# Kernel tuning notes

Hardware: AMD Instinct MI355X
Metric: run time of the kernel (lower is better)

## Reference

```python
import jax, jax.numpy as jnp
import numpy as np

B, L, D = 8, 8192, 256
H = 4 * D
EPS_LN = 1e-5
EPS_RELU = 1e-6
MIN_A, MAX_A, OFFSET = 0, 3, 3


def setup_inputs() -> dict:
    key = jax.random.key(0)
    ks = jax.random.split(key, 6)
    def n(k, shape, s=0.02):
        return jax.random.normal(k, shape, jnp.float32) * s
    return {
        "x": jax.random.normal(ks[0], (B, L, D), jnp.float32),
        "g1": jnp.ones((D,), jnp.float32), "b1": jnp.zeros((D,), jnp.float32),
        "g2": jnp.ones((D,), jnp.float32), "b2": jnp.zeros((D,), jnp.float32),
        "filt_w": n(ks[1], (L, D)),
        "w1": n(ks[2], (D, H)), "bb1": jnp.zeros((H,), jnp.float32),
        "w2": n(ks[3], (H, D)), "bb2": jnp.zeros((D,), jnp.float32),
    }


def layernorm(x, g, b):
    m = jnp.mean(x, -1, keepdims=True)
    v = jnp.var(x, -1, keepdims=True)
    return (x - m) * jax.lax.rsqrt(v + EPS_LN) * g + b


def maxpool_same(x, w):
    # stride-1 max pool over the last (frequency) axis, SAME padding
    if w == 1:
        return x
    return jax.lax.reduce_window(x, -jnp.inf, jax.lax.max,
                                 (1, 1, w), (1, 1, 1), "SAME")


def spsd1d(xt):
    """SPSD1D: FFT-based multi-scale (alpha) max-pooling spectral filter.
    xt: (B, D, L). Keeps rfft bins that are local maxima at every scale
    2**alpha for alpha in [MIN_A, MAX_A]; the lowest OFFSET bins pass through.
    Returns filtered signal (B, D, L) and argmax-alpha holder (B, D, F)."""
    X = jnp.fft.rfft(xt, axis=-1)              # (B, D, F), F = L//2 + 1
    mag = jnp.abs(X)
    pooled = jnp.stack([maxpool_same(mag, 2 ** a)
                        for a in range(MIN_A, MAX_A + 1)], 0)  # (A, B, D, F)
    max_holder = jnp.argmax(pooled, axis=0)
    env = jnp.max(pooled, axis=0)
    keep = (mag >= env) | (jnp.arange(mag.shape[-1]) < OFFSET)
    Xf = jnp.where(keep, X, 0.0)
    out = jnp.fft.irfft(Xf, n=xt.shape[-1], axis=-1)
    return out, max_holder


def _block_forward(x, g1, b1, g2, b2, filt_w, w1, bb1, w2, bb2):
    # EpsilonReLU(LayerNorm(x))
    h = jax.nn.relu(layernorm(x, g1, b1)) + EPS_RELU      # (B, L, D)
    # GlobalSPSDFilter: spsd over sequence axis, then elementwise weight
    f, _max_holder = spsd1d(jnp.swapaxes(h, 1, 2))        # (B, D, L)
    x0 = jnp.swapaxes(f, 1, 2) * filt_w                   # (B, L, D)
    # MLP(LayerNorm(x0)); dropouts are identity in eval mode
    m = layernorm(x0, g2, b2)
    m = jax.nn.gelu(m @ w1 + bb1, approximate=False)
    x0 = m @ w2 + bb2
    return x + x0


def reference(x, g1, b1, g2, b2, filt_w, w1, bb1, w2, bb2):
    return _block_forward(x, g1, b1, g2, b2, filt_w, w1, bb1, w2, bb2)
```

## Files before the change

### kernel.cpp

```cpp
#include <hip/hip_runtime.h>
#include <hip/hip_bf16.h>

#define BSZ  8
#define LSEQ 8192
#define DDIM 256
#define HDIM 1024
#define MFFT 4096

typedef __bf16 bf16;
typedef __bf16 bf16x8 __attribute__((ext_vector_type(8)));
typedef __bf16 bf16x4 __attribute__((ext_vector_type(4)));
typedef float  f32x4  __attribute__((ext_vector_type(4)));

__device__ __forceinline__ void wave_reduce2(float& a, float& b) {
    #pragma unroll
    for (int off = 1; off < 64; off <<= 1) {
        a += __shfl_xor(a, off);
        b += __shfl_xor(b, off);
    }
}

__device__ __forceinline__ void gl_lds16(const void* g, void* l) {
    __builtin_amdgcn_global_load_lds(
        (const __attribute__((address_space(1))) unsigned int*)(unsigned long long)g,
        (__attribute__((address_space(3))) unsigned int*)(unsigned int)(unsigned long long)l,
        16, 0, 0);
}

__global__ __launch_bounds__(256) void k0_prep(const float* __restrict__ w1,
                                               const float* __restrict__ w2,
                                               bf16* __restrict__ w1k,
                                               bf16* __restrict__ w2k,
                                               float2* __restrict__ tbl) {
    const int e = blockIdx.x * 256 + threadIdx.x;
    {
        const int c = e >> 13, r = e & 8191;
        const int ks = r >> 10, grp = (r >> 8) & 3, hh = (r >> 3) & 31, j = r & 7;
        w1k[e] = (bf16)w1[(ks * 32 + grp * 8 + j) * HDIM + c * 32 + hh];
    }
    {
        const int c = e >> 13, r = e & 8191;
        const int grp = r >> 11, d = (r >> 3) & 255, j = r & 7;
        w2k[e] = (bf16)w2[(c * 32 + grp * 8 + j) * DDIM + d];
    }
    if (e <= 8184) {
        float ang;
        if (e < 3584) {
            const int f = e / 512 + 1, jj = e & 511;
            ang = -6.283185307179586f * (float)(f * jj) * (1.0f / 4096.0f);
        } else if (e < 4032) {
            const int t = e - 3584, f = t / 64 + 1, jj = t & 63;
            ang = -6.283185307179586f * (float)(f * jj) * (1.0f / 512.0f);
        } else if (e < 4088) {
            const int t = e - 4032, f = t / 8 + 1, jj = t & 7;
            ang = -6.283185307179586f * (float)(f * jj) * (1.0f / 64.0f);
        } else {
            const int k = e - 4088;
            ang = 3.14159265358979323846f * (float)k * (1.0f / 4096.0f);
        }
        tbl[e] = make_float2(cosf(ang), sinf(ang));
    }
}

__global__ __launch_bounds__(256) void k1_ln1_relu_T(const float* __restrict__ x,
                                                     const float* __restrict__ g1,
                                                     const float* __restrict__ b1,
                                                     float* __restrict__ ht) {
    __shared__ float tile[DDIM][33];
    const int tid  = threadIdx.x;
    const int wave = tid >> 6, lane = tid & 63;
    const int b  = blockIdx.x >> 8;
    const int l0 = (blockIdx.x & 255) << 5;
    const float4 g4 = *(const float4*)&g1[lane * 4];
    const float4 b4 = *(const float4*)&b1[lane * 4];
    for (int r8 = 0; r8 < 8; ++r8) {
        const int l = r8 * 4 + wave;
        const float4 v = *(const float4*)&x[(b * LSEQ + l0 + l) * DDIM + lane * 4];
        float s = v.x + v.y + v.z + v.w;
        float q = v.x * v.x + v.y * v.y + v.z * v.z + v.w * v.w;
        wave_reduce2(s, q);
        const float mean = s * (1.0f / 256.0f);
        const float var  = q * (1.0f / 256.0f) - mean * mean;
        const float rstd = rsqrtf(var + 1e-5f);
        const float vv[4] = {v.x, v.y, v.z, v.w};
        const float gg[4] = {g4.x, g4.y, g4.z, g4.w};
        const float bb[4] = {b4.x, b4.y, b4.z, b4.w};
        #pragma unroll
        for (int j = 0; j < 4; ++j) {
            float t = (vv[j] - mean) * rstd * gg[j] + bb[j];
            t = fmaxf(t, 0.0f) + 1e-6f;
            tile[lane * 4 + j][l] = t;
        }
    }
    __syncthreads();
    for (int i = tid; i < DDIM * 32; i += 256) {
        const int d = i >> 5, ll = i & 31;
        ht[(b * DDIM + d) * LSEQ + l0 + ll] = tile[d][ll];
    }
}

__device__ __forceinline__ int zs(int p) { return p ^ ((p >> 4) & 15); }
__device__ __forceinline__ float2 cmulf(float2 a, float2 b) {
    return make_float2(fmaf(a.x, b.x, -a.y * b.y), fmaf(a.x, b.y, a.y * b.x));
}
__device__ __forceinline__ float2 f2add(float2 a, float2 b) { return make_float2(a.x + b.x, a.y + b.y); }
__device__ __forceinline__ float2 f2sub(float2 a, float2 b) { return make_float2(a.x - b.x, a.y - b.y); }
#define CSQ2 0.70710678118654752440f

__device__ __forceinline__ void dft8(float2 a0, float2 a1, float2 a2, float2 a3,
                                     float2 a4, float2 a5, float2 a6, float2 a7,
                                     float2& y0, float2& y1, float2& y2, float2& y3,
                                     float2& y4, float2& y5, float2& y6, float2& y7) {
    const float2 s0 = f2add(a0, a4), s1 = f2add(a1, a5), s2 = f2add(a2, a6), s3 = f2add(a3, a7);
    const float2 d0 = f2sub(a0, a4), d1 = f2sub(a1, a5), d2 = f2sub(a2, a6), d3 = f2sub(a3, a7);
    const float2 d1t = make_float2(CSQ2 * (d1.x + d1.y), CSQ2 * (d1.y - d1.x));
    const float2 d2t = make_float2(d2.y, -d2.x);
    const float2 d3t = make_float2(CSQ2 * (d3.y - d3.x), -CSQ2 * (d3.x + d3.y));
    const float2 u0 = f2add(s0, s2), u1 = f2add(s1, s3);
    const float2 v0 = f2sub(s0, s2);
    const float2 sd = f2sub(s1, s3);
    const float2 v1 = make_float2(sd.y, -sd.x);
    const float2 e0 = f2add(d0, d2t), e1 = f2add(d1t, d3t);
    const float2 f0 = f2sub(d0, d2t);
    const float2 dd = f2sub(d1t, d3t);
    const float2 f1 = make_float2(dd.y, -dd.x);
    y0 = f2add(u0, u1); y4 = f2sub(u0, u1);
    y2 = f2add(v0, v1); y6 = f2sub(v0, v1);
    y1 = f2add(e0, e1); y5 = f2sub(e0, e1);
    y3 = f2add(f0, f1); y7 = f2sub(f0, f1);
}

template<int LQ, int TOFF>
__device__ __forceinline__ void stage8(float2* Z, const float2* __restrict__ tw, int tid) {
    const int q = 1 << LQ;
    const int j = tid & (q - 1);
    const int base = ((tid >> LQ) << (LQ + 3)) + j;
    const float2 a0 = Z[zs(base)],         a1 = Z[zs(base + q)];
    const float2 a2 = Z[zs(base + 2 * q)], a3 = Z[zs(base + 3 * q)];
    const float2 a4 = Z[zs(base + 4 * q)], a5 = Z[zs(base + 5 * q)];
    const float2 a6 = Z[zs(base + 6 * q)], a7 = Z[zs(base + 7 * q)];
    float2 y0, y1, y2, y3, y4, y5, y6, y7;
    dft8(a0, a1, a2, a3, a4, a5, a6, a7, y0, y1, y2, y3, y4, y5, y6, y7);
    y1 = cmulf(y1, tw[TOFF + j]);
    y2 = cmulf(y2, tw[TOFF + q + j]);
    y3 = cmulf(y3, tw[TOFF + 2 * q + j]);
    y4 = cmulf(y4, tw[TOFF + 3 * q + j]);
    y5 = cmulf(y5, tw[TOFF + 4 * q + j]);
    y6 = cmulf(y6, tw[TOFF + 5 * q + j]);
    y7 = cmulf(y7, tw[TOFF + 6 * q + j]);
    Z[zs(base)]         = y0;
    Z[zs(base + 4 * q)] = y1;
    Z[zs(base + 2 * q)] = y2;
    Z[zs(base + 6 * q)] = y3;
    Z[zs(base + q)]     = y4;
    Z[zs(base + 5 * q)] = y5;
    Z[zs(base + 3 * q)] = y6;
    Z[zs(base + 7 * q)] = y7;
    __syncthreads();
}

__device__ __forceinline__ void stage8_last(float2* Z, int tid) {
    const int base = tid << 3;
    const float2 a0 = Z[zs(base)],     a1 = Z[zs(base + 1)];
    const float2 a2 = Z[zs(base + 2)], a3 = Z[zs(base + 3)];
    const float2 a4 = Z[zs(base + 4)], a5 = Z[zs(base + 5)];
    const float2 a6 = Z[zs(base + 6)], a7 = Z[zs(base + 7)];
    __syncthreads();
    float2 y0, y1, y2, y3, y4, y5, y6, y7;
    dft8(a0, a1, a2, a3, a4, a5, a6, a7, y0, y1, y2, y3, y4, y5, y6, y7);
    const int r9 = (int)(__brev((unsigned)tid) >> 23);
    Z[zs(r9)]        = y0;
    Z[zs(512 + r9)]  = y1;
    Z[zs(1024 + r9)] = y2;
    Z[zs(1536 + r9)] = y3;
    Z[zs(2048 + r9)] = y4;
    Z[zs(2560 + r9)] = y5;
    Z[zs(3072 + r9)] = y6;
    Z[zs(3584 + r9)] = y7;
    __syncthreads();
}

__device__ __forceinline__ void fft4096(float2* Z, const float2* __restrict__ tw, int tid) {
    stage8<9, 0>(Z, tw, tid);
    stage8<6, 3584>(Z, tw, tid);
    stage8<3, 4032>(Z, tw, tid);
    stage8_last(Z, tid);
}

__global__ __launch_bounds__(512, 4) void k2_spsd(float* __restrict__ ht,
                                                  const float2* __restrict__ tw) {
    __shared__ float2 Z[MFFT];
    __shared__ float  mg[MFFT + 1];
    const int tid = threadIdx.x;
    float* row = ht + (size_t)blockIdx.x * LSEQ;
    const float2* U = tw + 4088;

    for (int m = tid; m < MFFT; m += 512)
        Z[zs(m)] = *(const float2*)&row[2 * m];
    __syncthreads();

    fft4096(Z, tw, tid);

    for (int k = tid; k <= MFFT; k += 512) {
        const int ka = k & (MFFT - 1);
        const int kb = (MFFT - k) & (MFFT - 1);
        const float2 A = Z[zs(ka)], Bc = Z[zs(kb)];
        const float zex = 0.5f * (A.x + Bc.x), zey = 0.5f * (A.y - Bc.y);
        const float zox = 0.5f * (A.y + Bc.y), zoy = -0.5f * (A.x - Bc.x);
        const float2 u = U[k];
        const float cs = u.x, sn = -u.y;
        const float xr = zex + zox * cs - zoy * sn;
        const float xi = zey + zox * sn + zoy * cs;
        mg[k] = sqrtf(xr * xr + xi * xi);
    }
    __syncthreads();

    for (int k = tid; k <= 2048; k += 512) {
        const int km = (MFFT - k) & (MFFT - 1);
        const float2 Pk = Z[zs(k)];
        const float2 Pm = Z[zs(km)];
        const float2 u = U[k];
        const float cs = u.x, sn = u.y;
        const float zex = 0.5f * (Pk.x + Pm.x), zey = 0.5f * (Pk.y - Pm.y);
        const float zox = 0.5f * (Pk.y + Pm.y), zoy = -0.5f * (Pk.x - Pm.x);
        float xkr = zex + zox * cs + zoy * sn;
        float xki = zey - zox * sn + zoy * cs;
        const float zex2 = 0.5f * (Pm.x + Pk.x), zey2 = 0.5f * (Pm.y - Pk.y);
        const float zox2 = 0.5f * (Pm.y + Pk.y), zoy2 = -0.5f * (Pm.x - Pk.x);
        float xmr = zex2 - zox2 * cs + zoy2 * sn;
        float xmi = zey2 - zox2 * sn - zoy2 * cs;
        const int jm = MFFT - k;
        bool keepk, keepm;
        {
            const int lo = (k - 3 < 0) ? 0 : k - 3;
            const int hi = (k + 4 > 4096) ? 4096 : k + 4;
            float mx = mg[k];
            for (int t2 = lo; t2 <= hi; ++t2) mx = fmaxf(mx, mg[t2]);
            keepk = (k < 3) || (mg[k] >= mx);
        }
        {
            const int hi = (jm + 4 > 4096) ? 4096 : jm + 4;
            float mx = mg[jm];
            for (int t2 = jm - 3; t2 <= hi; ++t2) mx = fmaxf(mx, mg[t2]);
            keepm = (mg[jm] >= mx);
        }
        if (!keepk) { xkr = 0.0f; xki = 0.0f; }
        if (!keepm) { xmr = 0.0f; xmi = 0.0f; }
        const float zpex = 0.5f * (xkr + xmr), zpey = 0.5f * (xki - xmi);
        const float dfx  = 0.5f * (xkr - xmr), dfy  = 0.5f * (xki + xmi);
        const float zpox = dfx * cs - dfy * sn, zpoy = dfx * sn + dfy * cs;
        const float2 zk = make_float2(zpex - zpoy, zpey + zpox);
        const float zex3 = 0.5f * (xmr + xkr), zey3 = 0.5f * (xmi - xki);
        const float df2x = 0.5f * (xmr - xkr), df2y = 0.5f * (xmi + xki);
        const float zo3x = -df2x * cs - df2y * sn, zo3y = df2x * sn - df2y * cs;
        const float2 zm = make_float2(zex3 - zo3y, zey3 + zo3x);
        Z[zs(k)] = make_float2(zk.x, -zk.y);
        if (k != 0 && k != 2048) Z[zs(MFFT - k)] = make_float2(zm.x, -zm.y);
    }
    __syncthreads();

    fft4096(Z, tw, tid);

    const float invM = 1.0f / (float)MFFT;
    for (int m = tid; m < MFFT; m += 512) {
        const float2 z = Z[zs(m)];
        *(float2*)&row[2 * m] = make_float2(z.x * invM, -z.y * invM);
    }
}

__global__ __launch_bounds__(256) void k3_filt_ln2(const float* __restrict__ ht,
                                                   const float* __restrict__ fw,
                                                   const float* __restrict__ g2,
                                                   const float* __restrict__ b2,
                                                   bf16* __restrict__ aln) {
    __shared__ float tile[DDIM][33];
    const int tid  = threadIdx.x;
    const int wave = tid >> 6, lane = tid & 63;
    const int b  = blockIdx.x >> 8;
    const int l0 = (blockIdx.x & 255) << 5;
    for (int i = tid; i < DDIM * 32; i += 256) {
        const int d = i >> 5, ll = i & 31;
        tile[d][ll] = ht[(b * DDIM + d) * LSEQ + l0 + ll];
    }
    __syncthreads();
    const float4 g4 = *(const float4*)&g2[lane * 4];
    const float4 bb4 = *(const float4*)&b2[lane * 4];
    for (int r8 = 0; r8 < 8; ++r8) {
        const int l = r8 * 4 + wave;
        const int gl = l0 + l;
        const float4 f4 = *(const float4*)&fw[gl * DDIM + lane * 4];
        float v[4];
        v[0] = tile[lane * 4 + 0][l] * f4.x;
        v[1] = tile[lane * 4 + 1][l] * f4.y;
        v[2] = tile[lane * 4 + 2][l] * f4.z;
        v[3] = tile[lane * 4 + 3][l] * f4.w;
        float s = v[0] + v[1] + v[2] + v[3];
        float q = v[0] * v[0] + v[1] * v[1] + v[2] * v[2] + v[3] * v[3];
        wave_reduce2(s, q);
        const float mean = s * (1.0f / 256.0f);
        const float var  = q * (1.0f / 256.0f) - mean * mean;
        const float rstd = rsqrtf(var + 1e-5f);
        const float gg[4] = {g4.x, g4.y, g4.z, g4.w};
        const float bb[4] = {bb4.x, bb4.y, bb4.z, bb4.w};
        bf16x4 o;
        #pragma unroll
        for (int j = 0; j < 4; ++j)
            o[j] = (bf16)((v[j] - mean) * rstd * gg[j] + bb[j]);
        *(bf16x4*)&aln[(b * LSEQ + gl) * DDIM + lane * 4] = o;
    }
}

#define LDS_W1 0
#define LDS_W2 16384
#define LDS_LM 32768
#define LDS_TOT 40960

__global__ __launch_bounds__(512, 2) void k4_mlp(const bf16* __restrict__ aln,
                                                 const bf16* __restrict__ w1k,
                                                 const bf16* __restrict__ w2k,
                                                 const float* __restrict__ bb1,
                                                 const float* __restrict__ bb2,
                                                 const float* __restrict__ x,
                                                 float* __restrict__ out) {
    extern __shared__ char sm[];
    const int tid = threadIdx.x;
    const int lane = tid & 63, w = tid >> 6;
    const int rowLane = lane & 15, grp = lane >> 4;
    const int wm = w >> 1, wn = w & 1;
    const int row0 = blockIdx.x << 7;

    bf16x8 aF[2][8];
    #pragma unroll
    for (int fm = 0; fm < 2; ++fm) {
        const size_t rb = (size_t)(row0 + wm * 32 + fm * 16 + rowLane) * DDIM;
        #pragma unroll
        for (int ks = 0; ks < 8; ++ks)
            aF[fm][ks] = *(const bf16x8*)(aln + rb + ks * 32 + grp * 8);
    }
    {
        const char* g1 = (const char*)w1k;
        gl_lds16(g1 + tid * 16, sm + LDS_W1 + tid * 16);
        gl_lds16(g1 + 8192 + tid * 16, sm + LDS_W1 + 8192 + tid * 16);
    }
    __syncthreads();

    f32x4 acc[2][8];
    #pragma unroll
    for (int i = 0; i < 2; ++i)
        #pragma unroll
        for (int j2 = 0; j2 < 8; ++j2) acc[i][j2] = (f32x4){0.f, 0.f, 0.f, 0.f};

    for (int c = 0; c < 32; ++c) {
        {
            const char* g2 = (const char*)(w2k + (size_t)c * 8192);
            gl_lds16(g2 + tid * 16, sm + LDS_W2 + tid * 16);
            gl_lds16(g2 + 8192 + tid * 16, sm + LDS_W2 + 8192 + tid * 16);
        }
        const int hc = wn * 16 + rowLane;
        const float bias = bb1[c * 32 + hc];

        f32x4 p0 = {0.f, 0.f, 0.f, 0.f}, p1 = p0;
        #pragma unroll
        for (int ks = 0; ks < 8; ++ks) {
            const bf16x8 bF = *(const bf16x8*)(sm + LDS_W1 + ks * 2048 + grp * 512 + hc * 16);
            p0 = __builtin_amdgcn_mfma_f32_16x16x32_bf16(aF[0][ks], bF, p0, 0, 0, 0);
            p1 = __builtin_amdgcn_mfma_f32_16x16x32_bf16(aF[1][ks], bF, p1, 0, 0, 0);
        }
        const int kg = wn * 2 + (rowLane >> 3);
        const int cb = (rowLane & 7) * 2;
        #pragma unroll
        for (int fm = 0; fm < 2; ++fm) {
            const f32x4 pv = fm ? p1 : p0;
            #pragma unroll
            for (int j = 0; j < 4; ++j) {
                const int prow = wm * 32 + fm * 16 + grp * 4 + j;
                const float v = pv[j] + bias;
                const float ge = 0.5f * v * (1.0f + erff(v * 0.70710678118654752f));
                *(bf16*)(sm + LDS_LM + kg * 2048 + prow * 16 + cb) = (bf16)ge;
            }
        }
        __syncthreads();
        if (c < 31) {
            const char* g1 = (const char*)(w1k + (size_t)(c + 1) * 8192);
            gl_lds16(g1 + tid * 16, sm + LDS_W1 + tid * 16);
            gl_lds16(g1 + 8192 + tid * 16, sm + LDS_W1 + 8192 + tid * 16);
        }
        const int ar = wm * 32 + rowLane;
        const bf16x8 a0 = *(const bf16x8*)(sm + LDS_LM + grp * 2048 + ar * 16);
        const bf16x8 a1 = *(const bf16x8*)(sm + LDS_LM + grp * 2048 + (ar + 16) * 16);
        #pragma unroll
        for (int fn = 0; fn < 8; ++fn) {
            const int dcol = wn * 128 + fn * 16 + rowLane;
            const bf16x8 bw = *(const bf16x8*)(sm + LDS_W2 + grp * 4096 + dcol * 16);
            acc[0][fn] = __builtin_amdgcn_mfma_f32_16x16x32_bf16(a0, bw, acc[0][fn], 0, 0, 0);
            acc[1][fn] = __builtin_amdgcn_mfma_f32_16x16x32_bf16(a1, bw, acc[1][fn], 0, 0, 0);
        }
        __syncthreads();
    }
    #pragma unroll
    for (int fn = 0; fn < 8; ++fn) {
        const int dcol = wn * 128 + fn * 16 + rowLane;
        const float b2v = bb2[dcol];
        #pragma unroll
        for (int fm = 0; fm < 2; ++fm)
        #pragma unroll
        for (int j = 0; j < 4; ++j) {
            const int orow = row0 + wm * 32 + fm * 16 + grp * 4 + j;
            const int gi = orow * DDIM + dcol;
            out[gi] = acc[fm][fn][j] + b2v + x[gi];
        }
    }
}

extern "C" void kernel_launch(void* const* d_in, const int* in_sizes, int n_in,
                              void* d_out, int out_size, void* d_ws, size_t ws_size,
                              hipStream_t stream) {
    (void)in_sizes; (void)n_in; (void)out_size; (void)ws_size;
    const float* x   = (const float*)d_in[0];
    const float* g1  = (const float*)d_in[1];
    const float* b1  = (const float*)d_in[2];
    const float* g2  = (const float*)d_in[3];
    const float* b2  = (const float*)d_in[4];
    const float* fw  = (const float*)d_in[5];
    const float* w1  = (const float*)d_in[6];
    const float* bb1 = (const float*)d_in[7];
    const float* w2  = (const float*)d_in[8];
    const float* bb2 = (const float*)d_in[9];
    float* out = (float*)d_out;
    char*  ws  = (char*)d_ws;

    bf16*   aln = (bf16*)ws;
    bf16*   w1k = (bf16*)(ws + (size_t)33554432);
    bf16*   w2k = (bf16*)(ws + (size_t)34078720);
    float2* tbl = (float2*)(ws + (size_t)34603008);
    float* ht = out;

    k0_prep<<<dim3(1024), dim3(256), 0, stream>>>(w1, w2, w1k, w2k, tbl);
    k1_ln1_relu_T<<<dim3(2048), dim3(256), 0, stream>>>(x, g1, b1, ht);
    k2_spsd<<<dim3(2048), dim3(512), 0, stream>>>(ht, tbl);
    k3_filt_ln2<<<dim3(2048), dim3(256), 0, stream>>>(ht, fw, g2, b2, aln);
    k4_mlp<<<dim3(512), dim3(512), LDS_TOT, stream>>>(aln, w1k, w2k, bb1, bb2, x, out);
}
```

Baseline: 259.1 us.

## Halve MLP row tile to 64 and swizzle the GELU LDS buffer

The fused MLP kernel now handles 64 rows per block instead of 128, with 1024 blocks, half the per-thread accumulators and A fragments, and launch bounds raised to 4 blocks per CU. The intermediate GELU tile in LDS is re-laid out with an 80-byte row stride and an XOR swizzle to avoid bank conflicts, and total LDS shrinks. The aim is more parallelism and occupancy to hide latency, at the cost of loading each W1/W2 chunk twice as often across blocks and fewer MFMAs per LDS weight read.

```diff
diff --git a/kernel.cpp b/kernel.cpp
--- a/kernel.cpp
+++ b/kernel.cpp
@@ -313,9 +313,9 @@
 #define LDS_W1 0
 #define LDS_W2 16384
 #define LDS_LM 32768
-#define LDS_TOT 40960
-
-__global__ __launch_bounds__(512, 2) void k4_mlp(const bf16* __restrict__ aln,
+#define LDS_TOT 37888
+
+__global__ __launch_bounds__(512, 4) void k4_mlp(const bf16* __restrict__ aln,
                                                  const bf16* __restrict__ w1k,
                                                  const bf16* __restrict__ w2k,
                                                  const float* __restrict__ bb1,
@@ -327,15 +327,14 @@
     const int lane = tid & 63, w = tid >> 6;
     const int rowLane = lane & 15, grp = lane >> 4;
     const int wm = w >> 1, wn = w & 1;
-    const int row0 = blockIdx.x << 7;
-
-    bf16x8 aF[2][8];
-    #pragma unroll
-    for (int fm = 0; fm < 2; ++fm) {
-        const size_t rb = (size_t)(row0 + wm * 32 + fm * 16 + rowLane) * DDIM;
+    const int row0 = blockIdx.x << 6;
+
+    bf16x8 aF[8];
+    {
+        const size_t rb = (size_t)(row0 + wm * 16 + rowLane) * DDIM;
         #pragma unroll
         for (int ks = 0; ks < 8; ++ks)
-            aF[fm][ks] = *(const bf16x8*)(aln + rb + ks * 32 + grp * 8);
+            aF[ks] = *(const bf16x8*)(aln + rb + ks * 32 + grp * 8);
     }
     {
         const char* g1 = (const char*)w1k;
@@ -344,40 +343,32 @@
     }
     __syncthreads();
 
-    f32x4 acc[2][8];
+    f32x4 acc[8];
     #pragma unroll
-    for (int i = 0; i < 2; ++i)
-        #pragma unroll
-        for (int j2 = 0; j2 < 8; ++j2) acc[i][j2] = (f32x4){0.f, 0.f, 0.f, 0.f};
+    for (int i = 0; i < 8; ++i) acc[i] = (f32x4){0.f, 0.f, 0.f, 0.f};
 
     for (int c = 0; c < 32; ++c) {
         {
-            const char* g2 = (const char*)(w2k + (size_t)c * 8192);
-            gl_lds16(g2 + tid * 16, sm + LDS_W2 + tid * 16);
-            gl_lds16(g2 + 8192 + tid * 16, sm + LDS_W2 + 8192 + tid * 16);
+            const char* g2p = (const char*)(w2k + (size_t)c * 8192);
+            gl_lds16(g2p + tid * 16, sm + LDS_W2 + tid * 16);
+            gl_lds16(g2p + 8192 + tid * 16, sm + LDS_W2 + 8192 + tid * 16);
         }
         const int hc = wn * 16 + rowLane;
         const float bias = bb1[c * 32 + hc];
 
-        f32x4 p0 = {0.f, 0.f, 0.f, 0.f}, p1 = p0;
+        f32x4 p = {0.f, 0.f, 0.f, 0.f};
         #pragma unroll
         for (int ks = 0; ks < 8; ++ks) {
             const bf16x8 bF = *(const bf16x8*)(sm + LDS_W1 + ks * 2048 + grp * 512 + hc * 16);
-            p0 = __builtin_amdgcn_mfma_f32_16x16x32_bf16(aF[0][ks], bF, p0, 0, 0, 0);
-            p1 = __builtin_amdgcn_mfma_f32_16x16x32_bf16(aF[1][ks], bF, p1, 0, 0, 0);
-        }
-        const int kg = wn * 2 + (rowLane >> 3);
-        const int cb = (rowLane & 7) * 2;
-        #pragma unroll
-        for (int fm = 0; fm < 2; ++fm) {
-            const f32x4 pv = fm ? p1 : p0;
-            #pragma unroll
-            for (int j = 0; j < 4; ++j) {
-                const int prow = wm * 32 + fm * 16 + grp * 4 + j;
-                const float v = pv[j] + bias;
-                const float ge = 0.5f * v * (1.0f + erff(v * 0.70710678118654752f));
-                *(bf16*)(sm + LDS_LM + kg * 2048 + prow * 16 + cb) = (bf16)ge;
-            }
+            p = __builtin_amdgcn_mfma_f32_16x16x32_bf16(aF[ks], bF, p, 0, 0, 0);
+        }
+        const int hs = hc >> 3, hb = (hc & 7) * 2;
+        #pragma unroll
+        for (int j = 0; j < 4; ++j) {
+            const int prow = wm * 16 + grp * 4 + j;
+            const float v = p[j] + bias;
+            const float ge = 0.5f * v * (1.0f + erff(v * 0.70710678118654752f));
+            *(bf16*)(sm + LDS_LM + prow * 80 + ((hs ^ (prow & 3)) * 16) + hb) = (bf16)ge;
         }
         __syncthreads();
         if (c < 31) {
@@ -385,15 +376,13 @@
             gl_lds16(g1 + tid * 16, sm + LDS_W1 + tid * 16);
             gl_lds16(g1 + 8192 + tid * 16, sm + LDS_W1 + 8192 + tid * 16);
         }
-        const int ar = wm * 32 + rowLane;
-        const bf16x8 a0 = *(const bf16x8*)(sm + LDS_LM + grp * 2048 + ar * 16);
-        const bf16x8 a1 = *(const bf16x8*)(sm + LDS_LM + grp * 2048 + (ar + 16) * 16);
+        const int ar = wm * 16 + rowLane;
+        const bf16x8 aM = *(const bf16x8*)(sm + LDS_LM + ar * 80 + ((grp ^ (ar & 3)) * 16));
         #pragma unroll
         for (int fn = 0; fn < 8; ++fn) {
             const int dcol = wn * 128 + fn * 16 + rowLane;
             const bf16x8 bw = *(const bf16x8*)(sm + LDS_W2 + grp * 4096 + dcol * 16);
-            acc[0][fn] = __builtin_amdgcn_mfma_f32_16x16x32_bf16(a0, bw, acc[0][fn], 0, 0, 0);
-            acc[1][fn] = __builtin_amdgcn_mfma_f32_16x16x32_bf16(a1, bw, acc[1][fn], 0, 0, 0);
+            acc[fn] = __builtin_amdgcn_mfma_f32_16x16x32_bf16(aM, bw, acc[fn], 0, 0, 0);
         }
         __syncthreads();
     }
@@ -402,12 +391,10 @@
         const int dcol = wn * 128 + fn * 16 + rowLane;
         const float b2v = bb2[dcol];
         #pragma unroll
-        for (int fm = 0; fm < 2; ++fm)
-        #pragma unroll
         for (int j = 0; j < 4; ++j) {
-            const int orow = row0 + wm * 32 + fm * 16 + grp * 4 + j;
+            const int orow = row0 + wm * 16 + grp * 4 + j;
             const int gi = orow * DDIM + dcol;
-            out[gi] = acc[fm][fn][j] + b2v + x[gi];
+            out[gi] = acc[fn][j] + b2v + x[gi];
         }
     }
 }
@@ -439,5 +426,5 @@
     k1_ln1_relu_T<<<dim3(2048), dim3(256), 0, stream>>>(x, g1, b1, ht);
     k2_spsd<<<dim3(2048), dim3(512), 0, stream>>>(ht, tbl);
     k3_filt_ln2<<<dim3(2048), dim3(256), 0, stream>>>(ht, fw, g2, b2, aln);
-    k4_mlp<<<dim3(512), dim3(512), LDS_TOT, stream>>>(aln, w1k, w2k, bb1, bb2, x, out);
-}
+    k4_mlp<<<dim3(1024), dim3(512), LDS_TOT, stream>>>(aln, w1k, w2k, bb1, bb2, x, out);
+}
```

After: 248.1 us. -4.2%, faster.

## Retile MLP kernel to 64-row blocks with 64-wide hidden chunks

Applied to the files above, without the earlier changes.

Changes the fused MLP kernel from 128-row tiles with 32-wide hidden chunks to 64-row tiles with 64-wide hidden chunks, arranging 8 waves as 2x4 instead of 4x2. Weight prepacking is reorganised to match, LDS grows to 72KB, and the grid doubles to 1024 blocks with half the accumulator registers per thread. The aim is more blocks in flight and fewer loop iterations and barriers. In exchange, each weight chunk is reused across fewer rows, so total weight traffic from L2 doubles, and the larger LDS footprint may limit occupancy.

```diff
diff --git a/kernel.cpp b/kernel.cpp
--- a/kernel.cpp
+++ b/kernel.cpp
@@ -34,14 +34,14 @@
                                                float2* __restrict__ tbl) {
     const int e = blockIdx.x * 256 + threadIdx.x;
     {
-        const int c = e >> 13, r = e & 8191;
-        const int ks = r >> 10, grp = (r >> 8) & 3, hh = (r >> 3) & 31, j = r & 7;
-        w1k[e] = (bf16)w1[(ks * 32 + grp * 8 + j) * HDIM + c * 32 + hh];
+        const int c = e >> 14, r = e & 16383;
+        const int ks = r >> 11, grp = (r >> 9) & 3, hh = (r >> 3) & 63, j = r & 7;
+        w1k[e] = (bf16)w1[(ks * 32 + grp * 8 + j) * HDIM + c * 64 + hh];
     }
     {
-        const int c = e >> 13, r = e & 8191;
-        const int grp = r >> 11, d = (r >> 3) & 255, j = r & 7;
-        w2k[e] = (bf16)w2[(c * 32 + grp * 8 + j) * DDIM + d];
+        const int c = e >> 14, r = e & 16383;
+        const int ks2 = r >> 13, grp = (r >> 11) & 3, d = (r >> 3) & 255, j = r & 7;
+        w2k[e] = (bf16)w2[(c * 64 + ks2 * 32 + grp * 8 + j) * DDIM + d];
     }
     if (e <= 8184) {
         float ang;
@@ -311,11 +311,11 @@
 }
 
 #define LDS_W1 0
-#define LDS_W2 16384
-#define LDS_LM 32768
-#define LDS_TOT 40960
-
-__global__ __launch_bounds__(512, 2) void k4_mlp(const bf16* __restrict__ aln,
+#define LDS_W2 32768
+#define LDS_LM 65536
+#define LDS_TOT 73728
+
+__global__ __launch_bounds__(512, 4) void k4_mlp(const bf16* __restrict__ aln,
                                                  const bf16* __restrict__ w1k,
                                                  const bf16* __restrict__ w2k,
                                                  const float* __restrict__ bb1,
@@ -326,8 +326,8 @@
     const int tid = threadIdx.x;
     const int lane = tid & 63, w = tid >> 6;
     const int rowLane = lane & 15, grp = lane >> 4;
-    const int wm = w >> 1, wn = w & 1;
-    const int row0 = blockIdx.x << 7;
+    const int wm = w >> 2, wn = w & 3;
+    const int row0 = blockIdx.x << 6;
 
     bf16x8 aF[2][8];
     #pragma unroll
@@ -339,35 +339,36 @@
     }
     {
         const char* g1 = (const char*)w1k;
-        gl_lds16(g1 + tid * 16, sm + LDS_W1 + tid * 16);
-        gl_lds16(g1 + 8192 + tid * 16, sm + LDS_W1 + 8192 + tid * 16);
-    }
-    __syncthreads();
-
-    f32x4 acc[2][8];
+        #pragma unroll
+        for (int r = 0; r < 4; ++r)
+            gl_lds16(g1 + r * 8192 + tid * 16, sm + LDS_W1 + r * 8192 + tid * 16);
+    }
+    __syncthreads();
+
+    f32x4 acc[2][4];
     #pragma unroll
     for (int i = 0; i < 2; ++i)
         #pragma unroll
-        for (int j2 = 0; j2 < 8; ++j2) acc[i][j2] = (f32x4){0.f, 0.f, 0.f, 0.f};
-
-    for (int c = 0; c < 32; ++c) {
+        for (int j2 = 0; j2 < 4; ++j2) acc[i][j2] = (f32x4){0.f, 0.f, 0.f, 0.f};
+
+    for (int c = 0; c < 16; ++c) {
         {
-            const char* g2 = (const char*)(w2k + (size_t)c * 8192);
-            gl_lds16(g2 + tid * 16, sm + LDS_W2 + tid * 16);
-            gl_lds16(g2 + 8192 + tid * 16, sm + LDS_W2 + 8192 + tid * 16);
+            const char* g2p = (const char*)w2k + (size_t)c * 32768;
+            #pragma unroll
+            for (int r = 0; r < 4; ++r)
+                gl_lds16(g2p + r * 8192 + tid * 16, sm + LDS_W2 + r * 8192 + tid * 16);
         }
         const int hc = wn * 16 + rowLane;
-        const float bias = bb1[c * 32 + hc];
+        const float bias = bb1[c * 64 + hc];
 
         f32x4 p0 = {0.f, 0.f, 0.f, 0.f}, p1 = p0;
         #pragma unroll
         for (int ks = 0; ks < 8; ++ks) {
-            const bf16x8 bF = *(const bf16x8*)(sm + LDS_W1 + ks * 2048 + grp * 512 + hc * 16);
+            const bf16x8 bF = *(const bf16x8*)(sm + LDS_W1 + ks * 4096 + grp * 1024 + hc * 16);
             p0 = __builtin_amdgcn_mfma_f32_16x16x32_bf16(aF[0][ks], bF, p0, 0, 0, 0);
             p1 = __builtin_amdgcn_mfma_f32_16x16x32_bf16(aF[1][ks], bF, p1, 0, 0, 0);
         }
-        const int kg = wn * 2 + (rowLane >> 3);
-        const int cb = (rowLane & 7) * 2;
+        const int plane = ((hc >> 5) * 4 + ((hc >> 3) & 3)) * 1024 + (hc & 7) * 2;
         #pragma unroll
         for (int fm = 0; fm < 2; ++fm) {
             const f32x4 pv = fm ? p1 : p0;
@@ -376,30 +377,33 @@
                 const int prow = wm * 32 + fm * 16 + grp * 4 + j;
                 const float v = pv[j] + bias;
                 const float ge = 0.5f * v * (1.0f + erff(v * 0.70710678118654752f));
-                *(bf16*)(sm + LDS_LM + kg * 2048 + prow * 16 + cb) = (bf16)ge;
+                *(bf16*)(sm + LDS_LM + plane + prow * 16) = (bf16)ge;
             }
         }
         __syncthreads();
-        if (c < 31) {
-            const char* g1 = (const char*)(w1k + (size_t)(c + 1) * 8192);
-            gl_lds16(g1 + tid * 16, sm + LDS_W1 + tid * 16);
-            gl_lds16(g1 + 8192 + tid * 16, sm + LDS_W1 + 8192 + tid * 16);
-        }
-        const int ar = wm * 32 + rowLane;
-        const bf16x8 a0 = *(const bf16x8*)(sm + LDS_LM + grp * 2048 + ar * 16);
-        const bf16x8 a1 = *(const bf16x8*)(sm + LDS_LM + grp * 2048 + (ar + 16) * 16);
-        #pragma unroll
-        for (int fn = 0; fn < 8; ++fn) {
-            const int dcol = wn * 128 + fn * 16 + rowLane;
-            const bf16x8 bw = *(const bf16x8*)(sm + LDS_W2 + grp * 4096 + dcol * 16);
-            acc[0][fn] = __builtin_amdgcn_mfma_f32_16x16x32_bf16(a0, bw, acc[0][fn], 0, 0, 0);
-            acc[1][fn] = __builtin_amdgcn_mfma_f32_16x16x32_bf16(a1, bw, acc[1][fn], 0, 0, 0);
+        if (c < 15) {
+            const char* g1 = (const char*)w1k + (size_t)(c + 1) * 32768;
+            #pragma unroll
+            for (int r = 0; r < 4; ++r)
+                gl_lds16(g1 + r * 8192 + tid * 16, sm + LDS_W1 + r * 8192 + tid * 16);
+        }
+        #pragma unroll
+        for (int ks2 = 0; ks2 < 2; ++ks2) {
+            const bf16x8 a0 = *(const bf16x8*)(sm + LDS_LM + (ks2 * 4 + grp) * 1024 + (wm * 32 + rowLane) * 16);
+            const bf16x8 a1 = *(const bf16x8*)(sm + LDS_LM + (ks2 * 4 + grp) * 1024 + (wm * 32 + 16 + rowLane) * 16);
+            #pragma unroll
+            for (int fn = 0; fn < 4; ++fn) {
+                const int dcol = wn * 64 + fn * 16 + rowLane;
+                const bf16x8 bw = *(const bf16x8*)(sm + LDS_W2 + (ks2 * 4 + grp) * 4096 + dcol * 16);
+                acc[0][fn] = __builtin_amdgcn_mfma_f32_16x16x32_bf16(a0, bw, acc[0][fn], 0, 0, 0);
+                acc[1][fn] = __builtin_amdgcn_mfma_f32_16x16x32_bf16(a1, bw, acc[1][fn], 0, 0, 0);
+            }
         }
         __syncthreads();
     }
     #pragma unroll
-    for (int fn = 0; fn < 8; ++fn) {
-        const int dcol = wn * 128 + fn * 16 + rowLane;
+    for (int fn = 0; fn < 4; ++fn) {
+        const int dcol = wn * 64 + fn * 16 + rowLane;
         const float b2v = bb2[dcol];
         #pragma unroll
         for (int fm = 0; fm < 2; ++fm)
@@ -439,5 +443,5 @@
     k1_ln1_relu_T<<<dim3(2048), dim3(256), 0, stream>>>(x, g1, b1, ht);
     k2_spsd<<<dim3(2048), dim3(512), 0, stream>>>(ht, tbl);
     k3_filt_ln2<<<dim3(2048), dim3(256), 0, stream>>>(ht, fw, g2, b2, aln);
-    k4_mlp<<<dim3(512), dim3(512), LDS_TOT, stream>>>(aln, w1k, w2k, bb1, bb2, x, out);
-}
+    k4_mlp<<<dim3(1024), dim3(512), LDS_TOT, stream>>>(aln, w1k, w2k, bb1, bb2, x, out);
+}
```

New measurement: 280.0 us. 8.1% more time.
